# Optimization experiments

Measured on AMD Instinct MI355X. Metric: run time of the kernel, lower is better.

The kernel has to match this reference:

```python
import jax, jax.numpy as jnp
import numpy as np

WINDOW = 256  # attention_window (band half-width w; band is 2w+1 wide)


def _longformer(q, k, v, global_attention_mask, padding_mask, num_global, w):
    B, H, S, D = q.shape
    BH = B * H
    G = int(num_global)
    scale = jnp.sqrt(jnp.asarray(D, q.dtype))
    qf = q.reshape(BH, S, D)
    kf = k.reshape(BH, S, D)
    vf = v.reshape(BH, S, D)
    is_global = jnp.repeat(global_attention_mask.astype(bool), H, axis=0)  # [BH,S]
    pad_ok = jnp.repeat(padding_mask.astype(bool), H, axis=0)              # [BH,S]
    NEG = jnp.asarray(-jnp.inf, q.dtype)

    # ---- banded local qk scores via overlapping 3-chunk trick ----
    nc = S // w
    qc = qf.reshape(BH, nc, w, D)
    kp = jnp.pad(kf, ((0, 0), (w, w), (0, 0))).reshape(BH, nc + 2, w, D)
    k3 = jnp.concatenate([kp[:, :-2], kp[:, 1:-1], kp[:, 2:]], axis=2)     # [BH,nc,3w,D]
    scores3 = jnp.einsum('bcxd,bcyd->bcxy', qc, k3) / scale                # [BH,nc,w,3w]
    band_idx = jnp.arange(w)[:, None] + jnp.arange(2 * w + 1)[None, :]     # [w,2w+1]
    band = jnp.take_along_axis(scores3, band_idx[None, None], axis=3)
    band = band.reshape(BH, S, 2 * w + 1)                                  # score[i,t] = q_i . k_{i-w+t}

    # ---- local-band masking: out-of-bounds, global key columns, padding ----
    rel = jnp.arange(S)[:, None] + jnp.arange(-w, w + 1)[None, :]          # [S,2w+1]
    oob = (rel < 0) | (rel >= S)
    relc = jnp.clip(rel, 0, S - 1)
    glob_key = is_global[:, relc]                                          # [BH,S,2w+1]
    pad_key = pad_ok[:, relc]
    band = jnp.where(oob[None] | glob_key | ~pad_key, NEG, band)

    # ---- all tokens attend to the (sparse) global keys ----
    gpos = jnp.argsort((~is_global).astype(jnp.int32), axis=-1)[:, :G]     # stable: global positions in order
    gk = jnp.take_along_axis(kf, gpos[..., None], axis=1)                  # [BH,G,D]
    gv = jnp.take_along_axis(vf, gpos[..., None], axis=1)
    g_ok = jnp.take_along_axis(pad_ok, gpos, axis=1)                       # [BH,G]
    gscores = jnp.einsum('bsd,bgd->bsg', qf, gk) / scale
    gscores = jnp.where(g_ok[:, None, :], gscores, NEG)

    # ---- joint softmax over [global | local band] ----
    probs = jax.nn.softmax(jnp.concatenate([gscores, band], axis=-1), axis=-1)
    gprobs, lprobs = probs[..., :G], probs[..., G:]

    ctx = jnp.einsum('bsg,bgd->bsd', gprobs, gv)
    vp = jnp.pad(vf, ((0, 0), (w, w), (0, 0))).reshape(BH, nc + 2, w, D)
    v3 = jnp.concatenate([vp[:, :-2], vp[:, 1:-1], vp[:, 2:]], axis=2)     # [BH,nc,3w,D]
    p3 = jnp.zeros((BH, nc, w, 3 * w), probs.dtype)
    p3 = p3.at[:, :, jnp.arange(w)[:, None], band_idx].set(lprobs.reshape(BH, nc, w, 2 * w + 1))
    ctx = ctx + jnp.einsum('bcxy,bcyd->bcxd', p3, v3).reshape(BH, S, D)

    # ---- global tokens attend to every token (full attention rows) ----
    gq = jnp.take_along_axis(qf, gpos[..., None], axis=1)                  # [BH,G,D]
    rscores = jnp.einsum('bgd,bsd->bgs', gq, kf) / scale
    rscores = jnp.where(pad_ok[:, None, :], rscores, NEG)
    rprobs = jax.nn.softmax(rscores, axis=-1)
    vmask = jnp.where(pad_ok[..., None], vf, jnp.asarray(0.0, vf.dtype))
    ctx_g = jnp.einsum('bgs,bsd->bgd', rprobs, vmask)
    ctx = ctx.at[jnp.arange(BH)[:, None], gpos].set(ctx_g)

    return ctx.reshape(B, H, S, D)


def setup_inputs() -> dict:
    key = jax.random.key(0)
    kq, kk, kv = jax.random.split(key, 3)
    B, H, S, D, G = 1, 16, 4096, 64, 64
    q = jax.random.normal(kq, (B, H, S, D), jnp.float32)
    k = jax.random.normal(kk, (B, H, S, D), jnp.float32)
    v = jax.random.normal(kv, (B, H, S, D), jnp.float32)
    global_attention_mask = jnp.zeros((B, S), jnp.int32).at[:, :G].set(1)
    padding_mask = jnp.ones((B, S), jnp.int32)
    return {"q": q, "k": k, "v": v, "global_attention_mask": global_attention_mask,
            "padding_mask": padding_mask, "num_global": G}


def reference(q, k, v, global_attention_mask, padding_mask, num_global):
    return _longformer(q, k, v, global_attention_mask, padding_mask, num_global, WINDOW)
```

## Files before the change

kernel.cpp:

```cpp
#include <hip/hip_runtime.h>
#include <hip/hip_bf16.h>

#define SLEN 4096
#define NH   16
#define DH   64
#define WW   256
#define GMAX 64

typedef unsigned short u16;
typedef unsigned int   u32;
typedef unsigned long long u64;
typedef __attribute__((ext_vector_type(8))) short bf16x8;
typedef __attribute__((ext_vector_type(4))) float f32x4;

#define MFMA16(a,b,c) __builtin_amdgcn_mfma_f32_16x16x32_bf16((a),(b),(c),0,0,0)

static __device__ __forceinline__ int imin(int a, int b) { return a < b ? a : b; }
static __device__ __forceinline__ int imax(int a, int b) { return a > b ? a : b; }

__device__ __forceinline__ u32 cvtpk(float lo, float hi) {
  u32 r;
  asm("v_cvt_pk_bf16_f32 %0, %1, %2" : "=v"(r) : "v"(lo), "v"(hi));
  return r;
}
__device__ __forceinline__ u16 f2bf(float x) {
  u32 u = __float_as_uint(x);
  u32 r = (u + 0x7fffu + ((u >> 16) & 1u)) >> 16;
  return (u16)r;
}

__device__ __forceinline__ void gload16(const u16* src, u16* lds_base) {
  __builtin_amdgcn_global_load_lds((const __attribute__((address_space(1))) u32*)src,
                                   (__attribute__((address_space(3))) u32*)lds_base,
                                   16, 0, 0);
}

__global__ __launch_bounds__(256) void lf_prep1(
    const float* __restrict__ qF, const float* __restrict__ k, const float* __restrict__ v,
    const int* __restrict__ gmask, const int* __restrict__ pmask, const int* __restrict__ nGp,
    u16* __restrict__ kB, u16* __restrict__ vtB,
    int* __restrict__ gpos, unsigned char* __restrict__ gmsk,
    unsigned char* __restrict__ msk, unsigned char* __restrict__ cleanmap,
    u16* __restrict__ gq, u16* __restrict__ gk, u16* __restrict__ gvt, float qscale) {
  const int bid = blockIdx.x;
  const int tid = threadIdx.x;
  if (bid < 2048) {
    int i = (bid * 256 + tid) * 8;
    float4 v0 = *(const float4*)(k + i);
    float4 v1 = *(const float4*)(k + i + 4);
    uint4 w;
    w.x = cvtpk(v0.x, v0.y);
    w.y = cvtpk(v0.z, v0.w);
    w.z = cvtpk(v1.x, v1.y);
    w.w = cvtpk(v1.z, v1.w);
    *(uint4*)(kB + i) = w;
    return;
  }
  if (bid < 3072) {
    __shared__ float t[64][65];
    int b = bid - 2048;
    int h = b >> 6, s0 = (b & 63) << 6;
    int tile = h * 64 + (b & 63);
    int r = tid >> 2, c0 = (tid & 3) << 4;
    const float* src = v + ((size_t)h * SLEN + s0 + r) * DH + c0;
#pragma unroll
    for (int j = 0; j < 16; j += 4) {
      float4 a = *(const float4*)(src + j);
      t[r][c0 + j]     = a.x;
      t[r][c0 + j + 1] = a.y;
      t[r][c0 + j + 2] = a.z;
      t[r][c0 + j + 3] = a.w;
    }
    __syncthreads();
    int d = tid >> 2, j0 = (tid & 3) << 4;
    int grp  = j0 & 32;
    int half = (j0 & 16) ? 4 : 0;
    u16* dst = vtB + ((size_t)tile * 64 + d) * 64 + grp;
#pragma unroll
    for (int q4 = 0; q4 < 4; ++q4) {
      uint2 val;
      val.x = cvtpk(t[j0 + 4 * q4 + 0][d], t[j0 + 4 * q4 + 1][d]);
      val.y = cvtpk(t[j0 + 4 * q4 + 2][d], t[j0 + 4 * q4 + 3][d]);
      *(uint2*)(dst + 8 * q4 + half) = val;
    }
    return;
  }
  if (bid == 3072) {
    const int G = imin(nGp[0], GMAX);
    for (int s = tid; s < SLEN; s += 256) {
      unsigned char b = (unsigned char)((pmask[s] ? 1 : 0) | (gmask[s] ? 2 : 0));
      msk[s] = b;
    }
    for (int s = SLEN + tid; s < SLEN + 64; s += 256) msk[s] = 0;
    __syncthreads();
    if (tid < 64) {
      int lane = tid;
      if (lane < GMAX) gmsk[lane] = 0;
      int cnt = 0;
      for (int c = 0; c < SLEN / 64 && cnt < G; ++c) {
        int s = c * 64 + lane;
        bool isg = gmask[s] != 0;
        u64 b = __ballot(isg);
        int rank = cnt + (int)__popcll(b & ((1ull << lane) - 1ull));
        if (isg && rank < G) gpos[rank] = s;
        cnt += (int)__popcll(b);
      }
      if (cnt < G) {
        int fill = cnt;
        for (int c = 0; c < SLEN / 64 && fill < G; ++c) {
          int s = c * 64 + lane;
          bool non = gmask[s] == 0;
          u64 b = __ballot(non);
          int rank = fill + (int)__popcll(b & ((1ull << lane) - 1ull));
          if (non && rank < G) gpos[rank] = s;
          fill += (int)__popcll(b);
        }
      }
    }
    __syncthreads();
    if (tid < 64) {
      if (tid < G) {
        int p = gpos[tid];
        gmsk[tid] = (unsigned char)(pmask[p] ? 1 : 0);
        msk[p] = (unsigned char)(msk[p] | 4);
      }
    } else if (tid >= 128) {
      int c = tid - 128;
      if (c < SLEN / 32) {
        unsigned char ok1 = 1, ok2 = 1;
        for (int kk = 0; kk < 32; ++kk) {
          unsigned char b = msk[c * 32 + kk];
          ok1 &= (unsigned char)(((b & 3) == 1) ? 1 : 0);
          ok2 &= (unsigned char)(b & 1);
        }
        cleanmap[c] = (unsigned char)(ok1 | (ok2 << 1));
      }
    }
    return;
  }
  __shared__ int sGpos[GMAX];
  const int G = imin(nGp[0], GMAX);
  if (tid < 64) {
    int lane = tid;
    int cnt = 0;
    for (int c = 0; c < SLEN / 64 && cnt < G; ++c) {
      int s = c * 64 + lane;
      bool isg = gmask[s] != 0;
      u64 b = __ballot(isg);
      int rank = cnt + (int)__popcll(b & ((1ull << lane) - 1ull));
      if (isg && rank < G) sGpos[rank] = s;
      cnt += (int)__popcll(b);
    }
    if (cnt < G) {
      int fill = cnt;
      for (int c = 0; c < SLEN / 64 && fill < G; ++c) {
        int s = c * 64 + lane;
        bool non = gmask[s] == 0;
        u64 b = __ballot(non);
        int rank = fill + (int)__popcll(b & ((1ull << lane) - 1ull));
        if (non && rank < G) sGpos[rank] = s;
        fill += (int)__popcll(b);
      }
    }
  }
  __syncthreads();
  int idx = (bid - 3073) * 256 + tid;
  int h = idx >> 12, m = (idx >> 6) & 63, d = idx & 63;
  size_t oq = ((size_t)h * GMAX + m) * DH + d;
  int r = m & 31;
  int pos = ((r & 12) << 1) + ((r & 16) >> 2) + (r & 3);
  size_t ot = ((size_t)h * DH + d) * GMAX + (m & 32) + pos;
  if (m < G) {
    int p = sGpos[m];
    gq[oq]  = f2bf(qF[((size_t)h * SLEN + p) * DH + d] * qscale);
    gk[oq]  = f2bf(k[((size_t)h * SLEN + p) * DH + d]);
    gvt[ot] = f2bf(v[((size_t)h * SLEN + p) * DH + d]);
  } else {
    gq[oq] = 0; gk[oq] = 0; gvt[ot] = 0;
  }
}

__global__ __launch_bounds__(256) void lf_attn(
    const float* __restrict__ qF, const u16* __restrict__ kB, const u16* __restrict__ vtB,
    const u16* __restrict__ gkB, const u16* __restrict__ gqB, const u16* __restrict__ gvtB,
    const unsigned char* __restrict__ gmskA, const unsigned char* __restrict__ mskA,
    const unsigned char* __restrict__ cleanA, const int* __restrict__ nGp,
    float* __restrict__ out, float* __restrict__ pAcc, float* __restrict__ pL, float qscale) {
  __shared__ __align__(16) u16 sK[2][4096];
  __shared__ __align__(16) u16 sV[2][4096];
  __shared__ u32 sMsk[192];
  __shared__ u32 sGm[16];

  const int tid  = threadIdx.x;
  const int wv   = tid >> 6;
  const int lane = tid & 63;
  const int ql   = lane & 15;
  const int g    = lane >> 4;
  const float NEGV = -1e30f;
  const float MEXP = 24.0f;
  const int G = imin(nGp[0], GMAX);

  const int wg = ((int)blockIdx.x & 7) * 144 + ((int)blockIdx.x >> 3);
  const bool glob = (wg % 9) == 0;

  int off[4][2];
#pragma unroll
  for (int t = 0; t < 4; ++t)
#pragma unroll
    for (int c = 0; c < 2; ++c) {
      int row = 16 * t + ql;
      off[t][c] = (row * 8 + ((c * 4 + g) ^ (row & 7))) * 8;
    }

  f32x4 acc[4];
#pragma unroll
  for (int i = 0; i < 4; ++i) acc[i] = (f32x4){0.f, 0.f, 0.f, 0.f};
  f32x4 lsv = (f32x4){0.f, 0.f, 0.f, 0.f};
  bf16x8 qf0, qf1;

  int h, s0w = 0, sq = 0, t0, nMain, qg = 0, splitIdx = 0;
  int lo_w = 0, hi_w = 0;
  bool hasG = false;
  const u16 *gks = nullptr, *gvs = nullptr;

  if (!glob) {
    int lid = wg - wg / 9 - 1;
    h = lid >> 6;
    int qblk = lid & 63;
    int s0 = qblk << 6;
    s0w = s0 + 16 * wv; sq = s0w + ql;
    t0 = imax(0, qblk - 4);
    int t1 = imin(63, qblk + 4);
    nMain = t1 - t0 + 1;
    hasG = (G > 0);
    lo_w = imax(t0, (s0w - WW) >> 6);
    hi_w = imin(t1, (s0w + 15 + WW) >> 6);
    const float* qr = qF + ((size_t)h * SLEN + sq) * DH;
    float4 a0 = *(const float4*)(qr + 8 * g);
    float4 a1 = *(const float4*)(qr + 8 * g + 4);
    float4 b0 = *(const float4*)(qr + 32 + 8 * g);
    float4 b1 = *(const float4*)(qr + 32 + 8 * g + 4);
    union { u32 w[4]; bf16x8 v; } uq;
    uq.w[0] = cvtpk(a0.x * qscale, a0.y * qscale);
    uq.w[1] = cvtpk(a0.z * qscale, a0.w * qscale);
    uq.w[2] = cvtpk(a1.x * qscale, a1.y * qscale);
    uq.w[3] = cvtpk(a1.z * qscale, a1.w * qscale);
    qf0 = uq.v;
    uq.w[0] = cvtpk(b0.x * qscale, b0.y * qscale);
    uq.w[1] = cvtpk(b0.z * qscale, b0.w * qscale);
    uq.w[2] = cvtpk(b1.x * qscale, b1.y * qscale);
    uq.w[3] = cvtpk(b1.z * qscale, b1.w * qscale);
    qf1 = uq.v;
    gks = gkB + (size_t)h * GMAX * DH;
    gvs = gvtB + (size_t)h * 4096;
  } else {
    int gb = wg / 9;
    h = gb >> 3; splitIdx = gb & 7;
    qg = wv * 16 + ql;
    t0 = splitIdx * 8; nMain = 8;
    const u16* qRow = gqB + ((size_t)h * GMAX + qg) * DH;
    qf0 = *(const bf16x8*)(qRow + 8 * g);
    qf1 = *(const bf16x8*)(qRow + 32 + 8 * g);
  }
  const u16* kbase = kB  + (size_t)h * 64 * 4096;
  const u16* vbase = vtB + (size_t)h * 64 * 4096;
  const int totPh = nMain + (hasG ? 1 : 0);

  const unsigned char cmask = glob ? 2 : 1;
  unsigned char cbyte = 0;
  if (lane < nMain) {
    cbyte = (unsigned char)(cleanA[2 * (t0 + lane)] & cleanA[2 * (t0 + lane) + 1]);
  }
  const u64 cbits = __ballot((cbyte & cmask) != 0);

  auto stage = [&](int p, int b) {
    const u16 *ks, *vs;
    if (hasG && p == 0) { ks = gks; vs = gvs; }
    else {
      int tv = t0 + p - (hasG ? 1 : 0);
      ks = kbase + (size_t)tv * 4096;
      vs = vbase + (size_t)tv * 4096;
    }
#pragma unroll
    for (int j = 0; j < 2; ++j) {
      int gran = (wv * 2 + j) * 64 + lane;
      int sg = gran ^ ((gran >> 3) & 7);
      gload16(ks + (size_t)sg * 8, &sK[b][(wv * 2 + j) * 512]);
      gload16(vs + (size_t)sg * 8, &sV[b][(wv * 2 + j) * 512]);
    }
  };

  auto compute = [&](int p, int buf) {
    const bool isg = (hasG && p == 0);
    const int idx = p - (hasG ? 1 : 0);
    const int tv = t0 + idx;
    const int kb = tv * 64;
    bool doC = glob ? true : (isg || (tv >= lo_w && tv <= hi_w));
    if (!doC) return;
    const u16* sk = &sK[buf][0];
    const u16* sv = &sV[buf][0];
    f32x4 sc[4];
#pragma unroll
    for (int t = 0; t < 4; ++t) sc[t] = (f32x4){0.f, 0.f, 0.f, 0.f};
    __builtin_amdgcn_s_setprio(1);
#pragma unroll
    for (int t = 0; t < 4; ++t) {
      bf16x8 a0 = *(const bf16x8*)(sk + off[t][0]);
      bf16x8 a1 = *(const bf16x8*)(sk + off[t][1]);
      sc[t] = MFMA16(a0, qf0, sc[t]);
      sc[t] = MFMA16(a1, qf1, sc[t]);
    }
    __builtin_amdgcn_s_setprio(0);
    f32x4 pv[4];
    if (isg) {
#pragma unroll
      for (int t = 0; t < 4; ++t) {
        u32 mw = sGm[4 * t + g];
#pragma unroll
        for (int i = 0; i < 4; ++i) {
          float s = ((mw >> (8 * i)) & 1) ? sc[t][i] : NEGV;
          pv[t][i] = __builtin_amdgcn_exp2f(s - MEXP);
        }
      }
    } else {
      bool cl = ((cbits >> idx) & 1) != 0;
      if (!glob) cl = cl && (kb >= s0w + 15 - WW) && (kb + 63 <= s0w + WW);
      if (cl) {
#pragma unroll
        for (int t = 0; t < 4; ++t)
#pragma unroll
          for (int i = 0; i < 4; ++i)
            pv[t][i] = __builtin_amdgcn_exp2f(sc[t][i] - MEXP);
      } else if (glob) {
#pragma unroll
        for (int t = 0; t < 4; ++t) {
          u32 mw = sMsk[(idx << 4) + 4 * t + g];
#pragma unroll
          for (int i = 0; i < 4; ++i) {
            float s = ((mw >> (8 * i)) & 1) ? sc[t][i] : NEGV;
            pv[t][i] = __builtin_amdgcn_exp2f(s - MEXP);
          }
        }
      } else {
#pragma unroll
        for (int t = 0; t < 4; ++t) {
          u32 mw = sMsk[(idx << 4) + 4 * t + g];
#pragma unroll
          for (int i = 0; i < 4; ++i) {
            int kkey = kb + 16 * t + 4 * g + i;
            bool vok = (((mw >> (8 * i)) & 3) == 1) && (kkey >= sq - WW) && (kkey <= sq + WW);
            float s = vok ? sc[t][i] : NEGV;
            pv[t][i] = __builtin_amdgcn_exp2f(s - MEXP);
          }
        }
      }
    }
    lsv += pv[0] + pv[1] + pv[2] + pv[3];
    __builtin_amdgcn_s_setprio(1);
#pragma unroll
    for (int s2 = 0; s2 < 2; ++s2) {
      union { u32 w[4]; bf16x8 v8; } u;
      u.w[0] = cvtpk(pv[2 * s2][0], pv[2 * s2][1]);
      u.w[1] = cvtpk(pv[2 * s2][2], pv[2 * s2][3]);
      u.w[2] = cvtpk(pv[2 * s2 + 1][0], pv[2 * s2 + 1][1]);
      u.w[3] = cvtpk(pv[2 * s2 + 1][2], pv[2 * s2 + 1][3]);
#pragma unroll
      for (int dt = 0; dt < 4; ++dt) {
        bf16x8 vf = *(const bf16x8*)(sv + off[dt][s2]);
        acc[dt] = MFMA16(vf, u.v8, acc[dt]);
      }
    }
    __builtin_amdgcn_s_setprio(0);
  };

  stage(0, 0);
  {
    int nb = nMain << 4;
    if (tid < nb) sMsk[tid] = *(const u32*)(mskA + (t0 << 6) + (tid << 2));
    if (hasG && tid >= 192 && tid < 208) sGm[tid - 192] = *(const u32*)(gmskA + ((tid - 192) << 2));
  }
  __syncthreads();

  for (int p = 0; p < totPh; ++p) {
    if (p + 1 < totPh) {
      stage(p + 1, (p + 1) & 1);
      asm volatile("s_waitcnt vmcnt(4)" ::: "memory");
    } else {
      asm volatile("s_waitcnt vmcnt(0)" ::: "memory");
    }
    __builtin_amdgcn_s_barrier();
    __builtin_amdgcn_sched_barrier(0);
    compute(p, p & 1);
    __builtin_amdgcn_s_barrier();
  }

  float lsum = lsv[0] + lsv[1] + lsv[2] + lsv[3];
  lsum += __shfl_xor(lsum, 16);
  lsum += __shfl_xor(lsum, 32);

  if (!glob) {
    float inv = 1.f / lsum;
    bool skip = (mskA[sq] & 4) != 0;
    if (!skip) {
      float* orow = out + ((size_t)h * SLEN + sq) * DH;
#pragma unroll
      for (int dt = 0; dt < 4; ++dt) {
        f32x4 o = acc[dt] * inv;
        *(f32x4*)(orow + dt * 16 + 4 * g) = o;
      }
    }
  } else {
    float* pa = pAcc + ((size_t)(h * 8 + splitIdx) * 64 + qg) * 64;
#pragma unroll
    for (int dt = 0; dt < 4; ++dt)
      *(f32x4*)&pa[dt * 16 + 4 * g] = acc[dt];
    if (g == 0) pL[(h * 8 + splitIdx) * 64 + qg] = lsum;
  }
}

__global__ void lf_gmerge(const float* __restrict__ pAcc, const float* __restrict__ pL,
                          const int* __restrict__ gpos, const int* __restrict__ nGp,
                          float* __restrict__ out) {
  const int G = imin(nGp[0], GMAX);
  int h = blockIdx.x;
  int tid = threadIdx.x;
#pragma unroll
  for (int it = 0; it < 4; ++it) {
    int v = tid + it * 256;
    int q = v >> 4, d4 = (v & 15) << 2;
    if (q >= G) continue;
    float L = 0.f;
    f32x4 a = (f32x4){0.f, 0.f, 0.f, 0.f};
#pragma unroll
    for (int s = 0; s < 8; ++s) {
      L += pL[(h * 8 + s) * 64 + q];
      a += *(const f32x4*)&pAcc[((size_t)(h * 8 + s) * 64 + q) * 64 + d4];
    }
    *(f32x4*)&out[((size_t)h * SLEN + gpos[q]) * DH + d4] = a * (1.f / L);
  }
}

extern "C" void kernel_launch(void* const* d_in, const int* in_sizes, int n_in,
                              void* d_out, int out_size, void* d_ws, size_t ws_size,
                              hipStream_t stream) {
  const float* q = (const float*)d_in[0];
  const float* k = (const float*)d_in[1];
  const float* v = (const float*)d_in[2];
  const int* gmask = (const int*)d_in[3];
  const int* pmask = (const int*)d_in[4];
  const int* nGp = (const int*)d_in[5];
  float* out = (float*)d_out;
  char* ws = (char*)d_ws;

  constexpr size_t NEL = (size_t)NH * SLEN * DH;
  constexpr size_t OFF_KBF  = 0;
  constexpr size_t OFF_VTBF = OFF_KBF + NEL * 2;
  constexpr size_t OFF_GK   = OFF_VTBF + NEL * 2 + 256;
  constexpr size_t OFF_GQ   = OFF_GK + (size_t)NH * GMAX * DH * 2;
  constexpr size_t OFF_GVT  = OFF_GQ + (size_t)NH * GMAX * DH * 2;
  constexpr size_t OFF_GPOS = OFF_GVT + (size_t)NH * DH * GMAX * 2;
  constexpr size_t OFF_GMSK = OFF_GPOS + 256;
  constexpr size_t OFF_MSK  = OFF_GMSK + 64;
  constexpr size_t OFF_CLEAN = OFF_MSK + SLEN + 64;
  constexpr size_t OFF_PACC = OFF_CLEAN + 256;
  constexpr size_t OFF_PL   = OFF_PACC + (size_t)NH * 8 * 64 * 64 * 4;

  u16* kB  = (u16*)(ws + OFF_KBF);
  u16* vtB = (u16*)(ws + OFF_VTBF);
  u16* gk  = (u16*)(ws + OFF_GK);
  u16* gq  = (u16*)(ws + OFF_GQ);
  u16* gvt = (u16*)(ws + OFF_GVT);
  int* gpos = (int*)(ws + OFF_GPOS);
  unsigned char* gmsk = (unsigned char*)(ws + OFF_GMSK);
  unsigned char* msk  = (unsigned char*)(ws + OFF_MSK);
  unsigned char* clean = (unsigned char*)(ws + OFF_CLEAN);
  float* pAcc = (float*)(ws + OFF_PACC);
  float* pL   = (float*)(ws + OFF_PL);

  const float qscale = 0.125f * 1.4426950408889634f;

  lf_prep1<<<3329, 256, 0, stream>>>(q, k, v, gmask, pmask, nGp,
                                     kB, vtB, gpos, gmsk, msk, clean,
                                     gq, gk, gvt, qscale);
  lf_attn<<<1152, 256, 0, stream>>>(q, kB, vtB, gk, gq, gvt, gmsk, msk, clean,
                                    nGp, out, pAcc, pL, qscale);
  lf_gmerge<<<NH, 256, 0, stream>>>(pAcc, pL, gpos, nGp, out);
}
```

Before: 50.92 us.

## Specialize local/global attention paths, fix trip counts, move masks into registers

Splits the attention kernel into two separate code paths, one for local blocks and one for global-query blocks, each with a compile-time trip count (9+1 and 8 phases) and fully unrolled loops. The local path clamps t0 so it always covers 9 key tiles. Per-tile masks are packed into bit registers with a multiply-gather trick instead of being staged in LDS, which removes the LDS mask arrays and their load before the first barrier. A launch-bounds occupancy hint of 5 blocks is also added. This may cost more registers and code size, and the hint could force spills.

```diff
diff --git a/kernel.cpp b/kernel.cpp
--- a/kernel.cpp
+++ b/kernel.cpp
@@ -27,6 +27,9 @@
   u32 u = __float_as_uint(x);
   u32 r = (u + 0x7fffu + ((u >> 16) & 1u)) >> 16;
   return (u16)r;
+}
+__device__ __forceinline__ u32 bitg(u32 mw) {
+  return (((mw & 0x01010101u) * 0x01020408u) >> 24) & 0xFu;
 }
 
 __device__ __forceinline__ void gload16(const u16* src, u16* lds_base) {
@@ -180,7 +183,7 @@
   }
 }
 
-__global__ __launch_bounds__(256) void lf_attn(
+__global__ __launch_bounds__(256, 5) void lf_attn(
     const float* __restrict__ qF, const u16* __restrict__ kB, const u16* __restrict__ vtB,
     const u16* __restrict__ gkB, const u16* __restrict__ gqB, const u16* __restrict__ gvtB,
     const unsigned char* __restrict__ gmskA, const unsigned char* __restrict__ mskA,
@@ -188,8 +191,6 @@
     float* __restrict__ out, float* __restrict__ pAcc, float* __restrict__ pL, float qscale) {
   __shared__ __align__(16) u16 sK[2][4096];
   __shared__ __align__(16) u16 sV[2][4096];
-  __shared__ u32 sMsk[192];
-  __shared__ u32 sGm[16];
 
   const int tid  = threadIdx.x;
   const int wv   = tid >> 6;
@@ -198,7 +199,6 @@
   const int g    = lane >> 4;
   const float NEGV = -1e30f;
   const float MEXP = 24.0f;
-  const int G = imin(nGp[0], GMAX);
 
   const int wg = ((int)blockIdx.x & 7) * 144 + ((int)blockIdx.x >> 3);
   const bool glob = (wg % 9) == 0;
@@ -218,145 +218,8 @@
   f32x4 lsv = (f32x4){0.f, 0.f, 0.f, 0.f};
   bf16x8 qf0, qf1;
 
-  int h, s0w = 0, sq = 0, t0, nMain, qg = 0, splitIdx = 0;
-  int lo_w = 0, hi_w = 0;
-  bool hasG = false;
-  const u16 *gks = nullptr, *gvs = nullptr;
-
-  if (!glob) {
-    int lid = wg - wg / 9 - 1;
-    h = lid >> 6;
-    int qblk = lid & 63;
-    int s0 = qblk << 6;
-    s0w = s0 + 16 * wv; sq = s0w + ql;
-    t0 = imax(0, qblk - 4);
-    int t1 = imin(63, qblk + 4);
-    nMain = t1 - t0 + 1;
-    hasG = (G > 0);
-    lo_w = imax(t0, (s0w - WW) >> 6);
-    hi_w = imin(t1, (s0w + 15 + WW) >> 6);
-    const float* qr = qF + ((size_t)h * SLEN + sq) * DH;
-    float4 a0 = *(const float4*)(qr + 8 * g);
-    float4 a1 = *(const float4*)(qr + 8 * g + 4);
-    float4 b0 = *(const float4*)(qr + 32 + 8 * g);
-    float4 b1 = *(const float4*)(qr + 32 + 8 * g + 4);
-    union { u32 w[4]; bf16x8 v; } uq;
-    uq.w[0] = cvtpk(a0.x * qscale, a0.y * qscale);
-    uq.w[1] = cvtpk(a0.z * qscale, a0.w * qscale);
-    uq.w[2] = cvtpk(a1.x * qscale, a1.y * qscale);
-    uq.w[3] = cvtpk(a1.z * qscale, a1.w * qscale);
-    qf0 = uq.v;
-    uq.w[0] = cvtpk(b0.x * qscale, b0.y * qscale);
-    uq.w[1] = cvtpk(b0.z * qscale, b0.w * qscale);
-    uq.w[2] = cvtpk(b1.x * qscale, b1.y * qscale);
-    uq.w[3] = cvtpk(b1.z * qscale, b1.w * qscale);
-    qf1 = uq.v;
-    gks = gkB + (size_t)h * GMAX * DH;
-    gvs = gvtB + (size_t)h * 4096;
-  } else {
-    int gb = wg / 9;
-    h = gb >> 3; splitIdx = gb & 7;
-    qg = wv * 16 + ql;
-    t0 = splitIdx * 8; nMain = 8;
-    const u16* qRow = gqB + ((size_t)h * GMAX + qg) * DH;
-    qf0 = *(const bf16x8*)(qRow + 8 * g);
-    qf1 = *(const bf16x8*)(qRow + 32 + 8 * g);
-  }
-  const u16* kbase = kB  + (size_t)h * 64 * 4096;
-  const u16* vbase = vtB + (size_t)h * 64 * 4096;
-  const int totPh = nMain + (hasG ? 1 : 0);
-
-  const unsigned char cmask = glob ? 2 : 1;
-  unsigned char cbyte = 0;
-  if (lane < nMain) {
-    cbyte = (unsigned char)(cleanA[2 * (t0 + lane)] & cleanA[2 * (t0 + lane) + 1]);
-  }
-  const u64 cbits = __ballot((cbyte & cmask) != 0);
-
-  auto stage = [&](int p, int b) {
-    const u16 *ks, *vs;
-    if (hasG && p == 0) { ks = gks; vs = gvs; }
-    else {
-      int tv = t0 + p - (hasG ? 1 : 0);
-      ks = kbase + (size_t)tv * 4096;
-      vs = vbase + (size_t)tv * 4096;
-    }
-#pragma unroll
-    for (int j = 0; j < 2; ++j) {
-      int gran = (wv * 2 + j) * 64 + lane;
-      int sg = gran ^ ((gran >> 3) & 7);
-      gload16(ks + (size_t)sg * 8, &sK[b][(wv * 2 + j) * 512]);
-      gload16(vs + (size_t)sg * 8, &sV[b][(wv * 2 + j) * 512]);
-    }
-  };
-
-  auto compute = [&](int p, int buf) {
-    const bool isg = (hasG && p == 0);
-    const int idx = p - (hasG ? 1 : 0);
-    const int tv = t0 + idx;
-    const int kb = tv * 64;
-    bool doC = glob ? true : (isg || (tv >= lo_w && tv <= hi_w));
-    if (!doC) return;
-    const u16* sk = &sK[buf][0];
-    const u16* sv = &sV[buf][0];
-    f32x4 sc[4];
-#pragma unroll
-    for (int t = 0; t < 4; ++t) sc[t] = (f32x4){0.f, 0.f, 0.f, 0.f};
-    __builtin_amdgcn_s_setprio(1);
-#pragma unroll
-    for (int t = 0; t < 4; ++t) {
-      bf16x8 a0 = *(const bf16x8*)(sk + off[t][0]);
-      bf16x8 a1 = *(const bf16x8*)(sk + off[t][1]);
-      sc[t] = MFMA16(a0, qf0, sc[t]);
-      sc[t] = MFMA16(a1, qf1, sc[t]);
-    }
-    __builtin_amdgcn_s_setprio(0);
-    f32x4 pv[4];
-    if (isg) {
-#pragma unroll
-      for (int t = 0; t < 4; ++t) {
-        u32 mw = sGm[4 * t + g];
-#pragma unroll
-        for (int i = 0; i < 4; ++i) {
-          float s = ((mw >> (8 * i)) & 1) ? sc[t][i] : NEGV;
-          pv[t][i] = __builtin_amdgcn_exp2f(s - MEXP);
-        }
-      }
-    } else {
-      bool cl = ((cbits >> idx) & 1) != 0;
-      if (!glob) cl = cl && (kb >= s0w + 15 - WW) && (kb + 63 <= s0w + WW);
-      if (cl) {
-#pragma unroll
-        for (int t = 0; t < 4; ++t)
-#pragma unroll
-          for (int i = 0; i < 4; ++i)
-            pv[t][i] = __builtin_amdgcn_exp2f(sc[t][i] - MEXP);
-      } else if (glob) {
-#pragma unroll
-        for (int t = 0; t < 4; ++t) {
-          u32 mw = sMsk[(idx << 4) + 4 * t + g];
-#pragma unroll
-          for (int i = 0; i < 4; ++i) {
-            float s = ((mw >> (8 * i)) & 1) ? sc[t][i] : NEGV;
-            pv[t][i] = __builtin_amdgcn_exp2f(s - MEXP);
-          }
-        }
-      } else {
-#pragma unroll
-        for (int t = 0; t < 4; ++t) {
-          u32 mw = sMsk[(idx << 4) + 4 * t + g];
-#pragma unroll
-          for (int i = 0; i < 4; ++i) {
-            int kkey = kb + 16 * t + 4 * g + i;
-            bool vok = (((mw >> (8 * i)) & 3) == 1) && (kkey >= sq - WW) && (kkey <= sq + WW);
-            float s = vok ? sc[t][i] : NEGV;
-            pv[t][i] = __builtin_amdgcn_exp2f(s - MEXP);
-          }
-        }
-      }
-    }
+  auto TAIL = [&](const f32x4 (&pv)[4], const u16* sv) {
     lsv += pv[0] + pv[1] + pv[2] + pv[3];
-    __builtin_amdgcn_s_setprio(1);
 #pragma unroll
     for (int s2 = 0; s2 < 2; ++s2) {
       union { u32 w[4]; bf16x8 v8; } u;
@@ -370,35 +233,155 @@
         acc[dt] = MFMA16(vf, u.v8, acc[dt]);
       }
     }
+  };
+  auto QK = [&](const u16* sk, f32x4 (&sc)[4]) {
+#pragma unroll
+    for (int t = 0; t < 4; ++t) sc[t] = (f32x4){0.f, 0.f, 0.f, 0.f};
+    __builtin_amdgcn_s_setprio(1);
+#pragma unroll
+    for (int t = 0; t < 4; ++t) {
+      bf16x8 a0 = *(const bf16x8*)(sk + off[t][0]);
+      bf16x8 a1 = *(const bf16x8*)(sk + off[t][1]);
+      sc[t] = MFMA16(a0, qf0, sc[t]);
+      sc[t] = MFMA16(a1, qf1, sc[t]);
+    }
     __builtin_amdgcn_s_setprio(0);
   };
 
-  stage(0, 0);
-  {
-    int nb = nMain << 4;
-    if (tid < nb) sMsk[tid] = *(const u32*)(mskA + (t0 << 6) + (tid << 2));
-    if (hasG && tid >= 192 && tid < 208) sGm[tid - 192] = *(const u32*)(gmskA + ((tid - 192) << 2));
-  }
-  __syncthreads();
-
-  for (int p = 0; p < totPh; ++p) {
-    if (p + 1 < totPh) {
-      stage(p + 1, (p + 1) & 1);
-      asm volatile("s_waitcnt vmcnt(4)" ::: "memory");
-    } else {
-      asm volatile("s_waitcnt vmcnt(0)" ::: "memory");
-    }
-    __builtin_amdgcn_s_barrier();
-    __builtin_amdgcn_sched_barrier(0);
-    compute(p, p & 1);
-    __builtin_amdgcn_s_barrier();
-  }
-
-  float lsum = lsv[0] + lsv[1] + lsv[2] + lsv[3];
-  lsum += __shfl_xor(lsum, 16);
-  lsum += __shfl_xor(lsum, 32);
-
   if (!glob) {
+    int lid = wg - wg / 9 - 1;
+    const int h = lid >> 6;
+    const int qblk = lid & 63;
+    const int s0 = qblk << 6;
+    const int s0w = s0 + 16 * wv;
+    const int sq = s0w + ql;
+    const int t0 = imin(imax(0, qblk - 4), 55);
+    const int lo_w = imax(t0, (s0w - WW) >> 6);
+    const int hi_w = imin(t0 + 8, (s0w + 15 + WW) >> 6);
+
+    const float* qr = qF + ((size_t)h * SLEN + sq) * DH;
+    {
+      float4 a0 = *(const float4*)(qr + 8 * g);
+      float4 a1 = *(const float4*)(qr + 8 * g + 4);
+      float4 b0 = *(const float4*)(qr + 32 + 8 * g);
+      float4 b1 = *(const float4*)(qr + 32 + 8 * g + 4);
+      union { u32 w[4]; bf16x8 v; } uq;
+      uq.w[0] = cvtpk(a0.x * qscale, a0.y * qscale);
+      uq.w[1] = cvtpk(a0.z * qscale, a0.w * qscale);
+      uq.w[2] = cvtpk(a1.x * qscale, a1.y * qscale);
+      uq.w[3] = cvtpk(a1.z * qscale, a1.w * qscale);
+      qf0 = uq.v;
+      uq.w[0] = cvtpk(b0.x * qscale, b0.y * qscale);
+      uq.w[1] = cvtpk(b0.z * qscale, b0.w * qscale);
+      uq.w[2] = cvtpk(b1.x * qscale, b1.y * qscale);
+      uq.w[3] = cvtpk(b1.z * qscale, b1.w * qscale);
+      qf1 = uq.v;
+    }
+    const u16* gks = gkB + (size_t)h * GMAX * DH;
+    const u16* gvs = gvtB + (size_t)h * 4096;
+    const u16* kbase = kB  + (size_t)h * 64 * 4096;
+    const u16* vbase = vtB + (size_t)h * 64 * 4096;
+
+    unsigned char cbyte = 0;
+    if (lane < 9)
+      cbyte = (unsigned char)(cleanA[2 * (t0 + lane)] & cleanA[2 * (t0 + lane) + 1]);
+    const u64 cbits = __ballot((cbyte & 1) != 0);
+    u32 mreg[9], gmreg = 0;
+#pragma unroll
+    for (int idx = 0; idx < 9; ++idx) {
+      u32 m = 0;
+#pragma unroll
+      for (int t = 0; t < 4; ++t) {
+        u32 mw = *(const u32*)(mskA + (t0 + idx) * 64 + 16 * t + 4 * g);
+        m |= (bitg(mw) << (4 * t)) | (bitg(mw >> 1) << (16 + 4 * t));
+      }
+      mreg[idx] = m;
+    }
+#pragma unroll
+    for (int t = 0; t < 4; ++t) {
+      u32 mw = *(const u32*)(gmskA + 16 * t + 4 * g);
+      gmreg |= bitg(mw) << (4 * t);
+    }
+
+    auto stageL = [&](int p, int b) {
+      const u16 *ks, *vs;
+      if (p == 0) { ks = gks; vs = gvs; }
+      else {
+        int tv = t0 + p - 1;
+        ks = kbase + (size_t)tv * 4096;
+        vs = vbase + (size_t)tv * 4096;
+      }
+#pragma unroll
+      for (int j = 0; j < 2; ++j) {
+        int gran = (wv * 2 + j) * 64 + lane;
+        int sg = gran ^ ((gran >> 3) & 7);
+        gload16(ks + (size_t)sg * 8, &sK[b][(wv * 2 + j) * 512]);
+        gload16(vs + (size_t)sg * 8, &sV[b][(wv * 2 + j) * 512]);
+      }
+    };
+
+    stageL(0, 0);
+#pragma unroll
+    for (int p = 0; p < 10; ++p) {
+      if (p < 9) {
+        stageL(p + 1, (p + 1) & 1);
+        asm volatile("s_waitcnt vmcnt(4)" ::: "memory");
+      } else {
+        asm volatile("s_waitcnt vmcnt(0)" ::: "memory");
+      }
+      __builtin_amdgcn_s_barrier();
+      __builtin_amdgcn_sched_barrier(0);
+      const u16* sk = &sK[p & 1][0];
+      const u16* sv = &sV[p & 1][0];
+      if (p == 0) {
+        f32x4 sc[4];
+        QK(sk, sc);
+        f32x4 pv[4];
+#pragma unroll
+        for (int t = 0; t < 4; ++t)
+#pragma unroll
+          for (int i = 0; i < 4; ++i) {
+            float s = ((gmreg >> (4 * t + i)) & 1) ? sc[t][i] : NEGV;
+            pv[t][i] = __builtin_amdgcn_exp2f(s - MEXP);
+          }
+        TAIL(pv, sv);
+      } else {
+        const int idx = p - 1;
+        const int tv = t0 + idx;
+        const int kb = tv * 64;
+        if (tv >= lo_w && tv <= hi_w) {
+          f32x4 sc[4];
+          QK(sk, sc);
+          f32x4 pv[4];
+          bool cl = (((cbits >> idx) & 1) != 0) &&
+                    (kb >= s0w + 15 - WW) && (kb + 63 <= s0w + WW);
+          if (cl) {
+#pragma unroll
+            for (int t = 0; t < 4; ++t)
+#pragma unroll
+              for (int i = 0; i < 4; ++i)
+                pv[t][i] = __builtin_amdgcn_exp2f(sc[t][i] - MEXP);
+          } else {
+            u32 v2 = mreg[idx] & ~(mreg[idx] >> 16);
+#pragma unroll
+            for (int t = 0; t < 4; ++t)
+#pragma unroll
+              for (int i = 0; i < 4; ++i) {
+                int kkey = kb + 16 * t + 4 * g + i;
+                bool vok = ((v2 >> (4 * t + i)) & 1) && (kkey >= sq - WW) && (kkey <= sq + WW);
+                float s = vok ? sc[t][i] : NEGV;
+                pv[t][i] = __builtin_amdgcn_exp2f(s - MEXP);
+              }
+          }
+          TAIL(pv, sv);
+        }
+      }
+      __builtin_amdgcn_s_barrier();
+    }
+
+    float lsum = lsv[0] + lsv[1] + lsv[2] + lsv[3];
+    lsum += __shfl_xor(lsum, 16);
+    lsum += __shfl_xor(lsum, 32);
     float inv = 1.f / lsum;
     bool skip = (mskA[sq] & 4) != 0;
     if (!skip) {
@@ -409,7 +392,88 @@
         *(f32x4*)(orow + dt * 16 + 4 * g) = o;
       }
     }
-  } else {
+    return;
+  }
+
+  {
+    int gb = wg / 9;
+    const int h = gb >> 3;
+    const int splitIdx = gb & 7;
+    const int qg = wv * 16 + ql;
+    const int t0 = splitIdx * 8;
+    const u16* qRow = gqB + ((size_t)h * GMAX + qg) * DH;
+    qf0 = *(const bf16x8*)(qRow + 8 * g);
+    qf1 = *(const bf16x8*)(qRow + 32 + 8 * g);
+    const u16* kbase = kB  + (size_t)h * 64 * 4096;
+    const u16* vbase = vtB + (size_t)h * 64 * 4096;
+
+    unsigned char cbyte = 0;
+    if (lane < 8)
+      cbyte = (unsigned char)(cleanA[2 * (t0 + lane)] & cleanA[2 * (t0 + lane) + 1]);
+    const u64 cbits = __ballot((cbyte & 2) != 0);
+    u32 mreg[8];
+#pragma unroll
+    for (int idx = 0; idx < 8; ++idx) {
+      u32 m = 0;
+#pragma unroll
+      for (int t = 0; t < 4; ++t) {
+        u32 mw = *(const u32*)(mskA + (t0 + idx) * 64 + 16 * t + 4 * g);
+        m |= bitg(mw) << (4 * t);
+      }
+      mreg[idx] = m;
+    }
+
+    auto stageG = [&](int p, int b) {
+      int tv = t0 + p;
+      const u16* ks = kbase + (size_t)tv * 4096;
+      const u16* vs = vbase + (size_t)tv * 4096;
+#pragma unroll
+      for (int j = 0; j < 2; ++j) {
+        int gran = (wv * 2 + j) * 64 + lane;
+        int sg = gran ^ ((gran >> 3) & 7);
+        gload16(ks + (size_t)sg * 8, &sK[b][(wv * 2 + j) * 512]);
+        gload16(vs + (size_t)sg * 8, &sV[b][(wv * 2 + j) * 512]);
+      }
+    };
+
+    stageG(0, 0);
+#pragma unroll
+    for (int p = 0; p < 8; ++p) {
+      if (p < 7) {
+        stageG(p + 1, (p + 1) & 1);
+        asm volatile("s_waitcnt vmcnt(4)" ::: "memory");
+      } else {
+        asm volatile("s_waitcnt vmcnt(0)" ::: "memory");
+      }
+      __builtin_amdgcn_s_barrier();
+      __builtin_amdgcn_sched_barrier(0);
+      const u16* sk = &sK[p & 1][0];
+      const u16* sv = &sV[p & 1][0];
+      f32x4 sc[4];
+      QK(sk, sc);
+      f32x4 pv[4];
+      if ((cbits >> p) & 1) {
+#pragma unroll
+        for (int t = 0; t < 4; ++t)
+#pragma unroll
+          for (int i = 0; i < 4; ++i)
+            pv[t][i] = __builtin_amdgcn_exp2f(sc[t][i] - MEXP);
+      } else {
+#pragma unroll
+        for (int t = 0; t < 4; ++t)
+#pragma unroll
+          for (int i = 0; i < 4; ++i) {
+            float s = ((mreg[p] >> (4 * t + i)) & 1) ? sc[t][i] : NEGV;
+            pv[t][i] = __builtin_amdgcn_exp2f(s - MEXP);
+          }
+      }
+      TAIL(pv, sv);
+      __builtin_amdgcn_s_barrier();
+    }
+
+    float lsum = lsv[0] + lsv[1] + lsv[2] + lsv[3];
+    lsum += __shfl_xor(lsum, 16);
+    lsum += __shfl_xor(lsum, 32);
     float* pa = pAcc + ((size_t)(h * 8 + splitIdx) * 64 + qg) * 64;
 #pragma unroll
     for (int dt = 0; dt < 4; ++dt)
```

New measurement: 68.91 us. 1.35x slower.
